# Optimization experiments

Hardware: AMD Instinct MI355X
Metric: run time of the kernel (lower is better)

Reference implementation:

```python
import jax, jax.numpy as jnp
import numpy as np

D_IN = 4096
NUM_HEADS = 32
HEAD_DIM = 128
NUM_KV = 8
GROUP = NUM_HEADS // NUM_KV
EPS = 1e-6
ROPE_BASE = 10000.0


def rms_norm(x, scale):
    # norm over last dim (head_dim), computed in fp32 as in torch ref
    var = jnp.mean(x * x, axis=-1, keepdims=True)
    return x * jax.lax.rsqrt(var + EPS) * scale


def rope_cos_sin(positions, dim):
    inv_freq = 1.0 / (ROPE_BASE ** (jnp.arange(0, dim, 2, dtype=jnp.float32) / dim))
    angles = positions.astype(jnp.float32)[:, None] * inv_freq[None, :]  # (N, dim/2)
    angles = jnp.concatenate([angles, angles], axis=-1)  # (N, dim)
    return jnp.cos(angles), jnp.sin(angles)


def apply_rope(t, cos, sin):
    # t: (N, heads, D); cos/sin: (N, D)
    half = t.shape[-1] // 2
    rot = jnp.concatenate([-t[..., half:], t[..., :half]], axis=-1)
    return t * cos[:, None, :] + rot * sin[:, None, :]


def setup_inputs() -> dict:
    key = jax.random.key(0)
    ks = jax.random.split(key, 6)
    B, S = 1, 2048
    x = jax.random.normal(ks[0], (B, S, D_IN), dtype=jnp.float32)
    positions = jnp.arange(B * S, dtype=jnp.int32)
    sc = 0.02
    Wq = jax.random.normal(ks[1], (D_IN, NUM_HEADS * HEAD_DIM), dtype=jnp.float32) * sc
    Wk = jax.random.normal(ks[2], (D_IN, NUM_KV * HEAD_DIM), dtype=jnp.float32) * sc
    Wv = jax.random.normal(ks[3], (D_IN, NUM_KV * HEAD_DIM), dtype=jnp.float32) * sc
    Wo = jax.random.normal(ks[4], (NUM_HEADS * HEAD_DIM, D_IN), dtype=jnp.float32) * sc
    q_scale = jnp.ones((HEAD_DIM,), dtype=jnp.float32)
    k_scale = jnp.ones((HEAD_DIM,), dtype=jnp.float32)
    return {"x": x, "positions": positions, "Wq": Wq, "Wk": Wk, "Wv": Wv,
            "Wo": Wo, "q_scale": q_scale, "k_scale": k_scale}


def reference(x, positions, Wq, Wk, Wv, Wo, q_scale, k_scale):
    B, S, _ = x.shape
    N = B * S
    xf = x.reshape(N, D_IN)
    q = (xf @ Wq).reshape(N, NUM_HEADS, HEAD_DIM)
    k = (xf @ Wk).reshape(N, NUM_KV, HEAD_DIM)
    v = (xf @ Wv).reshape(N, NUM_KV, HEAD_DIM)
    # QK RMSNorm over head_dim
    q = rms_norm(q, q_scale)
    k = rms_norm(k, k_scale)
    # RoPE (rotate-half)
    cos, sin = rope_cos_sin(positions, HEAD_DIM)
    q = apply_rope(q, cos, sin)
    k = apply_rope(k, cos, sin)
    # (B, KV, group, S, D) for q; (B, KV, S, D) for k, v  (GQA broadcast)
    q = q.reshape(B, S, NUM_KV, GROUP, HEAD_DIM).transpose(0, 2, 3, 1, 4)
    k = k.reshape(B, S, NUM_KV, HEAD_DIM).transpose(0, 2, 1, 3)
    v = v.reshape(B, S, NUM_KV, HEAD_DIM).transpose(0, 2, 1, 3)
    scale = 1.0 / jnp.sqrt(jnp.float32(HEAD_DIM))
    scores = jnp.einsum('bghsd,bgtd->bghst', q, k) * scale  # (B,KV,G,S,S)
    causal = jnp.tril(jnp.ones((S, S), dtype=bool))
    scores = jnp.where(causal[None, None, None, :, :], scores, jnp.finfo(scores.dtype).min)
    attn = jax.nn.softmax(scores, axis=-1)
    ctx = jnp.einsum('bghst,bgtd->bghsd', attn, v)  # (B,KV,G,S,D)
    ctx = ctx.transpose(0, 3, 1, 2, 4).reshape(B, S, NUM_HEADS * HEAD_DIM)
    return ctx @ Wo
```

## Files before the change

kernel.cpp:

```cpp
#include <hip/hip_runtime.h>

#define S_LEN 2048
#define DMODEL 4096
#define NQKV 6144

typedef unsigned short u16;
typedef __attribute__((ext_vector_type(8))) short bf16x8;
typedef __attribute__((ext_vector_type(8))) unsigned short u16x8;
typedef __attribute__((ext_vector_type(4))) float f32x4;

#define NEG_BIG (-3.0e38f)

__device__ __forceinline__ float bf2f(u16 h) {
    union { unsigned u; float f; } c; c.u = ((unsigned)h) << 16; return c.f;
}
__device__ __forceinline__ u16 f2bf(float x) {
    union { float f; unsigned u; } c; c.f = x;
    return (u16)((c.u + 0x7fffu + ((c.u >> 16) & 1u)) >> 16);
}

__device__ __forceinline__ void gload16(const void* g, void* l) {
    __builtin_amdgcn_global_load_lds(
        (const __attribute__((address_space(1))) void*)g,
        (__attribute__((address_space(3))) void*)l, 16, 0, 0);
}

__device__ __forceinline__ void barfence() {
    asm volatile("" ::: "memory");
    __builtin_amdgcn_s_barrier();
    asm volatile("" ::: "memory");
}

#define MFMA16(d, av, bv) d = __builtin_amdgcn_mfma_f32_16x16x32_bf16(av, bv, d, 0, 0, 0)

__global__ __launch_bounds__(256) void detect_dtype(const u16* __restrict__ probe,
                                                    int* __restrict__ flags) {
    __shared__ int bad_s;
    if (threadIdx.x == 0) bad_s = 0;
    __syncthreads();
    int bad = 0;
    for (int i = threadIdx.x; i < 16384; i += 256) {
        float v = bf2f(probe[i]);
        if (!(fabsf(v) < 1e6f)) bad = 1;
    }
    if (bad) atomicOr(&bad_s, 1);
    __syncthreads();
    if (threadIdx.x == 0) { flags[0] = bad_s; flags[1] = 0; }
}

__global__ __launch_bounds__(256) void conv_bf16(const void* __restrict__ src,
                                                 u16* __restrict__ dst, long n,
                                                 const int* __restrict__ flag) {
    const bool f32 = (*flag != 0);
    long i = (long)blockIdx.x * 256 + threadIdx.x;
    long stride = (long)gridDim.x * 256;
    for (; i < n; i += stride) {
        float v = f32 ? ((const float*)src)[i] : bf2f(((const u16*)src)[i]);
        dst[i] = f2bf(v);
    }
}

__global__ __launch_bounds__(256) void transpose_any(
        const void* __restrict__ src, long base_off, long sld, long szoff,
        u16* __restrict__ dst, long dld, long dzoff,
        const int* __restrict__ flag) {
    __shared__ alignas(16) u16 tile[32][33];
    const bool f32 = (*flag != 0);
    u16* d = dst + (long)blockIdx.z * dzoff;
    long soff = base_off + (long)blockIdx.z * szoff;
    int c0 = blockIdx.x * 32, r0 = blockIdx.y * 32;
    int tx = threadIdx.x & 31, ty = threadIdx.x >> 5;
    for (int i = 0; i < 32; i += 8) {
        long idx = soff + (long)(r0 + ty + i) * sld + c0 + tx;
        float v = f32 ? ((const float*)src)[idx] : bf2f(((const u16*)src)[idx]);
        tile[ty + i][tx] = f2bf(v);
    }
    __syncthreads();
    for (int i = 0; i < 32; i += 8)
        d[(long)(c0 + ty + i) * dld + r0 + tx] = tile[tx][ty + i];
}

__global__ __launch_bounds__(512, 2) void gemm_dp4_bf16(
        const u16* __restrict__ A, const u16* __restrict__ BT,
        u16* __restrict__ C, int K, int ldc) {
    __shared__ alignas(16) u16 smem[57344];
    const int tid = threadIdx.x;
    const int lane = tid & 63, wid = tid >> 6;
    const int wr = wid >> 2, wc = wid & 3;
    const int lm = lane & 15, lq = lane >> 4;
    const int m0 = blockIdx.y * 256, n0 = blockIdx.x * 192;

    const int srow = tid >> 3;
    const int sgrp = (tid & 7) ^ (srow & 7);
    const u16* aS = A  + (size_t)(m0 + srow) * K + sgrp * 8;
    const u16* bS = BT + (size_t)(n0 + srow) * K + sgrp * 8;
    u16* ldsA = smem + tid * 8;
    u16* ldsB = smem + 16384 + tid * 8;

    auto stA = [&](int bufi, int c, int kti) {
        gload16(aS + (size_t)c * 64 * K + (size_t)kti * 64, ldsA + bufi * 28672 + c * 4096);
    };
    auto stB = [&](int bufi, int c, int kti) {
        gload16(bS + (size_t)c * 64 * K + (size_t)kti * 64, ldsB + bufi * 28672 + c * 4096);
    };
    auto rdA = [&](const u16* buf, int mi, int ks) {
        int row = wr * 128 + mi * 16 + lm;
        return *(const bf16x8*)(const void*)(buf + row * 64 + (((ks * 4 + lq) ^ (row & 7)) << 3));
    };
    auto rdB = [&](const u16* buf, int ni, int ks) {
        int row = wc * 48 + ni * 16 + lm;
        return *(const bf16x8*)(const void*)(buf + 16384 + row * 64 + (((ks * 4 + lq) ^ (row & 7)) << 3));
    };

    const int NK = K >> 6;
    stB(0, 0, 0); stB(0, 1, 0); stB(0, 2, 0);
    stA(0, 0, 0); stA(0, 2, 0); stA(0, 1, 0); stA(0, 3, 0);

    f32x4 acc[8][3] = {};
    bf16x8 b[3][2], a[2][2];

#pragma unroll 2
    for (int kt = 0; kt < NK; ++kt) {
        const u16* buf = smem + (kt & 1) * 28672;
        const int nb = (kt & 1) ^ 1;
        const int kn = kt + 1;
        const bool more = kn < NK;

        asm volatile("s_waitcnt vmcnt(2)" ::: "memory");
        barfence();
#pragma unroll
        for (int ni = 0; ni < 3; ++ni)
#pragma unroll
            for (int ks = 0; ks < 2; ++ks) b[ni][ks] = rdB(buf, ni, ks);
#pragma unroll
        for (int q = 0; q < 2; ++q)
#pragma unroll
            for (int ks = 0; ks < 2; ++ks) a[q][ks] = rdA(buf, q, ks);
        if (more) { stB(nb, 0, kn); stB(nb, 1, kn); stB(nb, 2, kn); }
        __builtin_amdgcn_s_setprio(1);
#pragma unroll
        for (int q = 0; q < 2; ++q)
#pragma unroll
            for (int ni = 0; ni < 3; ++ni)
#pragma unroll
                for (int ks = 0; ks < 2; ++ks) MFMA16(acc[q][ni], a[q][ks], b[ni][ks]);
        __builtin_amdgcn_s_setprio(0);

#pragma unroll
        for (int q = 0; q < 2; ++q)
#pragma unroll
            for (int ks = 0; ks < 2; ++ks) a[q][ks] = rdA(buf, 2 + q, ks);
        if (more) { stA(nb, 0, kn); stA(nb, 2, kn); }
        __builtin_amdgcn_s_setprio(1);
#pragma unroll
        for (int q = 0; q < 2; ++q)
#pragma unroll
            for (int ni = 0; ni < 3; ++ni)
#pragma unroll
                for (int ks = 0; ks < 2; ++ks) MFMA16(acc[2 + q][ni], a[q][ks], b[ni][ks]);
        __builtin_amdgcn_s_setprio(0);

        if (more) { asm volatile("s_waitcnt vmcnt(5)" ::: "memory"); }
        else      { asm volatile("s_waitcnt vmcnt(0)" ::: "memory"); }
        barfence();
#pragma unroll
        for (int q = 0; q < 2; ++q)
#pragma unroll
            for (int ks = 0; ks < 2; ++ks) a[q][ks] = rdA(buf, 4 + q, ks);
        if (more) { stA(nb, 1, kn); stA(nb, 3, kn); }
        __builtin_amdgcn_s_setprio(1);
#pragma unroll
        for (int q = 0; q < 2; ++q)
#pragma unroll
            for (int ni = 0; ni < 3; ++ni)
#pragma unroll
                for (int ks = 0; ks < 2; ++ks) MFMA16(acc[4 + q][ni], a[q][ks], b[ni][ks]);
        __builtin_amdgcn_s_setprio(0);

#pragma unroll
        for (int q = 0; q < 2; ++q)
#pragma unroll
            for (int ks = 0; ks < 2; ++ks) a[q][ks] = rdA(buf, 6 + q, ks);
        __builtin_amdgcn_s_setprio(1);
#pragma unroll
        for (int q = 0; q < 2; ++q)
#pragma unroll
            for (int ni = 0; ni < 3; ++ni)
#pragma unroll
                for (int ks = 0; ks < 2; ++ks) MFMA16(acc[6 + q][ni], a[q][ks], b[ni][ks]);
        __builtin_amdgcn_s_setprio(0);
    }

#pragma unroll
    for (int mi = 0; mi < 8; ++mi)
#pragma unroll
        for (int ni = 0; ni < 3; ++ni) {
            int col  = n0 + wc * 48 + ni * 16 + lm;
            int rowb = m0 + wr * 128 + mi * 16 + lq * 4;
#pragma unroll
            for (int r = 0; r < 4; ++r)
                C[(size_t)(rowb + r) * ldc + col] = f2bf(acc[mi][ni][r]);
        }
}

__global__ __launch_bounds__(512, 2) void gemm_dp3_f32(
        const u16* __restrict__ A, const u16* __restrict__ BT,
        float* __restrict__ C, int K, int ldc) {
    __shared__ alignas(16) u16 smem[49152];
    const int tid = threadIdx.x;
    const int lane = tid & 63, wid = tid >> 6;
    const int wr = wid >> 1, wc = wid & 1;
    const int lm = lane & 15, lq = lane >> 4;
    const int m0 = blockIdx.y * 128, n0 = blockIdx.x * 256;

    const int srow = tid >> 3;
    const int sgrp = (tid & 7) ^ (srow & 7);
    const u16* aS = A  + (size_t)(m0 + srow) * K + sgrp * 8;
    const u16* bS = BT + (size_t)(n0 + srow) * K + sgrp * 8;
    u16* ldsA = smem + tid * 8;
    u16* ldsB = smem + 8192 + tid * 8;

    auto stA = [&](int bufi, int c, int kti) {
        gload16(aS + (size_t)c * 64 * K + (size_t)kti * 64, ldsA + bufi * 24576 + c * 4096);
    };
    auto stB = [&](int bufi, int c, int kti) {
        gload16(bS + (size_t)c * 64 * K + (size_t)kti * 64, ldsB + bufi * 24576 + c * 4096);
    };
    auto rdA = [&](const u16* buf, int mi, int ks) {
        int row = wr * 32 + mi * 16 + lm;
        return *(const bf16x8*)(const void*)(buf + row * 64 + (((ks * 4 + lq) ^ (row & 7)) << 3));
    };
    auto rdB = [&](const u16* buf, int ni, int ks) {
        int row = wc * 128 + ni * 16 + lm;
        return *(const bf16x8*)(const void*)(buf + 8192 + row * 64 + (((ks * 4 + lq) ^ (row & 7)) << 3));
    };

    const int NK = K >> 6;
    stA(0, 0, 0); stA(0, 1, 0); stB(0, 0, 0); stB(0, 2, 0);
    stB(0, 1, 0); stB(0, 3, 0);

    f32x4 acc[2][8] = {};
    bf16x8 a[2][2], b[4][2];

#pragma unroll 2
    for (int kt = 0; kt < NK; ++kt) {
        const u16* buf = smem + (kt & 1) * 24576;
        const int nb = (kt & 1) ^ 1;
        const int kn = kt + 1;
        const bool more = kn < NK;

        asm volatile("s_waitcnt vmcnt(2)" ::: "memory");
        barfence();
#pragma unroll
        for (int mi = 0; mi < 2; ++mi)
#pragma unroll
            for (int ks = 0; ks < 2; ++ks) a[mi][ks] = rdA(buf, mi, ks);
#pragma unroll
        for (int ni = 0; ni < 4; ++ni)
#pragma unroll
            for (int ks = 0; ks < 2; ++ks) b[ni][ks] = rdB(buf, ni, ks);
        if (more) { stA(nb, 0, kn); stA(nb, 1, kn); stB(nb, 0, kn); stB(nb, 2, kn); }
        __builtin_amdgcn_s_setprio(1);
#pragma unroll
        for (int mi = 0; mi < 2; ++mi)
#pragma unroll
            for (int ni = 0; ni < 4; ++ni)
#pragma unroll
                for (int ks = 0; ks < 2; ++ks) MFMA16(acc[mi][ni], a[mi][ks], b[ni][ks]);
        __builtin_amdgcn_s_setprio(0);

        if (more) { asm volatile("s_waitcnt vmcnt(4)" ::: "memory"); }
        else      { asm volatile("s_waitcnt vmcnt(0)" ::: "memory"); }
        barfence();
#pragma unroll
        for (int ni = 0; ni < 4; ++ni)
#pragma unroll
            for (int ks = 0; ks < 2; ++ks) b[ni][ks] = rdB(buf, 4 + ni, ks);
        if (more) { stB(nb, 1, kn); stB(nb, 3, kn); }
        __builtin_amdgcn_s_setprio(1);
#pragma unroll
        for (int mi = 0; mi < 2; ++mi)
#pragma unroll
            for (int ni = 0; ni < 4; ++ni)
#pragma unroll
                for (int ks = 0; ks < 2; ++ks) MFMA16(acc[mi][4 + ni], a[mi][ks], b[ni][ks]);
        __builtin_amdgcn_s_setprio(0);
    }

#pragma unroll
    for (int mi = 0; mi < 2; ++mi)
#pragma unroll
        for (int ni = 0; ni < 8; ++ni) {
            int col  = n0 + wc * 128 + ni * 16 + lm;
            int rowb = m0 + wr * 32 + mi * 16 + lq * 4;
#pragma unroll
            for (int r = 0; r < 4; ++r)
                C[(size_t)(rowb + r) * ldc + col] = acc[mi][ni][r];
        }
}

__global__ __launch_bounds__(256) void rms_rope(
        const u16* __restrict__ qkv, const int* __restrict__ pos,
        const u16* __restrict__ qs, const u16* __restrict__ kscale,
        u16* __restrict__ Qb, u16* __restrict__ Kb) {
    int w = threadIdx.x >> 6, lane = threadIdx.x & 63;
    int task = blockIdx.x * 4 + w;
    int h = task >> 11, row = task & 2047;
    int base = (h < 32) ? h * 128 : 4096 + (h - 32) * 128;
    const u16* src = qkv + (size_t)row * NQKV + base;
    float t0 = bf2f(src[lane]), t1 = bf2f(src[lane + 64]);
    float ss = t0 * t0 + t1 * t1;
    for (int m = 1; m < 64; m <<= 1) ss += __shfl_xor(ss, m);
    float inv = rsqrtf(ss * (1.0f / 128.0f) + 1e-6f);
    const u16* sc = (h < 32) ? qs : kscale;
    float n0 = t0 * inv * bf2f(sc[lane]);
    float n1 = t1 * inv * bf2f(sc[lane + 64]);
    float p = (float)pos[row];
    float ang = p * __expf(-(float)lane * (9.210340371976184f / 64.0f));
    float c = cosf(ang), s = sinf(ang);
    float o0 = n0 * c - n1 * s;
    float o1 = n1 * c + n0 * s;
    float mul = (h < 32) ? 0.08838834764831845f : 1.0f;
    u16* dst = (h < 32) ? (Qb + ((size_t)h * S_LEN + row) * 128)
                        : (Kb + ((size_t)(h - 32) * S_LEN + row) * 128);
    dst[lane] = f2bf(o0 * mul);
    dst[lane + 64] = f2bf(o1 * mul);
}

__global__ __launch_bounds__(256, 2) void flash_attn(
        const u16* __restrict__ Qb, const u16* __restrict__ Kb,
        const u16* __restrict__ VTb, u16* __restrict__ ctx) {
    const int h = blockIdx.y, kvh = h >> 2;
    const int tid = threadIdx.x, lane = tid & 63, w = tid >> 6;
    const int lm = lane & 15, lq = lane >> 4;
    const int swz = (lm & 7) << 3;
    __shared__ alignas(16) u16 smem[36864];
    u16* Psm = smem + 32768;
    const u16* Kh = Kb + (size_t)kvh * S_LEN * 128;
    const u16* Vh = VTb + (size_t)kvh * 128 * S_LEN;

    auto stageK = [&](int j) {
        for (int i = 0; i < 4; ++i) {
            int g = i * 256 + tid;
            int row = g >> 4, s = g & 15;
            int sp = (s & 8) | ((s ^ row) & 7);
            gload16(Kh + (size_t)(j * 64 + row) * 128 + sp * 8,
                    smem + (j & 1) * 8192 + (size_t)(i * 256 + w * 64) * 8);
        }
    };
    auto stageV = [&](int j) {
        for (int i = 0; i < 4; ++i) {
            int g = i * 256 + tid;
            int d = g >> 3, s = g & 7;
            int sp = s ^ (d & 7);
            gload16(Vh + (size_t)d * S_LEN + j * 64 + sp * 8,
                    smem + 16384 + (j & 1) * 8192 + (size_t)(i * 256 + w * 64) * 8);
        }
    };

    for (int pass = 0; pass < 2; ++pass) {
        const int t = pass ? (31 - blockIdx.x) : blockIdx.x;
        const u16* Qh = Qb + ((size_t)h * S_LEN + (size_t)t * 64) * 128;

        barfence();
        for (int i = 0; i < 4; ++i) {
            int g = i * 256 + tid;
            int row = g >> 4, s = g & 15;
            int sp = (s & 8) | ((s ^ row) & 7);
            gload16(Qh + (size_t)row * 128 + sp * 8,
                    smem + (size_t)(i * 256 + w * 64) * 8);
        }
        asm volatile("s_waitcnt vmcnt(0)" ::: "memory");
        barfence();
        bf16x8 aq[4];
        for (int ks = 0; ks < 4; ++ks)
            aq[ks] = *(const bf16x8*)(const void*)(
                smem + (((w * 16 + lm) * 128 + ks * 32 + lq * 8) ^ swz));
        asm volatile("s_waitcnt lgkmcnt(0)" ::: "memory");
        barfence();
        stageK(0); stageV(0);

        float mrow[4], lrow[4];
        f32x4 accO[8];
        const f32x4 zero = {0.f, 0.f, 0.f, 0.f};
        for (int r = 0; r < 4; ++r) { mrow[r] = NEG_BIG; lrow[r] = 0.f; }
        for (int di = 0; di < 8; ++di) accO[di] = zero;

        for (int j = 0; j <= t; ++j) {
            const u16* Kj = smem + (j & 1) * 8192;
            const u16* Vj = smem + 16384 + (j & 1) * 8192;
            if (j < t) {
                stageK(j + 1); stageV(j + 1);
                asm volatile("s_waitcnt vmcnt(8)" ::: "memory");
            } else {
                asm volatile("s_waitcnt vmcnt(0)" ::: "memory");
            }
            barfence();

            f32x4 sacc[4] = {};
            for (int ks = 0; ks < 4; ++ks) {
                bf16x8 kf[4];
                for (int ni = 0; ni < 4; ++ni)
                    kf[ni] = *(const bf16x8*)(const void*)(
                        Kj + (((ni * 16 + lm) * 128 + ks * 32 + lq * 8) ^ swz));
                for (int ni = 0; ni < 4; ++ni)
                    sacc[ni] = __builtin_amdgcn_mfma_f32_16x16x32_bf16(aq[ks], kf[ni], sacc[ni], 0, 0, 0);
            }

            if (j == t) {
                for (int ni = 0; ni < 4; ++ni) {
                    int col = ni * 16 + lm;
                    for (int r = 0; r < 4; ++r)
                        if (col > w * 16 + lq * 4 + r) sacc[ni][r] = NEG_BIG;
                }
            }

            for (int r = 0; r < 4; ++r) {
                float mx = fmaxf(fmaxf(sacc[0][r], sacc[1][r]),
                                 fmaxf(sacc[2][r], sacc[3][r]));
                for (int sft = 1; sft < 16; sft <<= 1) mx = fmaxf(mx, __shfl_xor(mx, sft));
                float mN = fmaxf(mrow[r], mx);
                float alpha = __expf(mrow[r] - mN);
                mrow[r] = mN;
                float psum = 0.f;
                int prow = w * 16 + lq * 4 + r;
                for (int ni = 0; ni < 4; ++ni) {
                    float pv = __expf(sacc[ni][r] - mN);
                    psum += pv;
                    Psm[prow * 64 + ((ni * 16 + lm) ^ ((prow & 7) << 3))] = f2bf(pv);
                }
                for (int sft = 1; sft < 16; sft <<= 1) psum += __shfl_xor(psum, sft);
                lrow[r] = lrow[r] * alpha + psum;
                for (int di = 0; di < 8; ++di) accO[di][r] *= alpha;
            }
            asm volatile("s_waitcnt lgkmcnt(0)" ::: "memory");
            barfence();

            for (int ks2 = 0; ks2 < 2; ++ks2) {
                bf16x8 pf = *(const bf16x8*)(const void*)(
                    Psm + (((w * 16 + lm) * 64 + ks2 * 32 + lq * 8) ^ swz));
                for (int di = 0; di < 8; ++di) {
                    bf16x8 vf = *(const bf16x8*)(const void*)(
                        Vj + (((di * 16 + lm) * 64 + ks2 * 32 + lq * 8) ^ swz));
                    accO[di] = __builtin_amdgcn_mfma_f32_16x16x32_bf16(pf, vf, accO[di], 0, 0, 0);
                }
            }
            barfence();
        }

        for (int r = 0; r < 4; ++r) {
            float invl = 1.0f / fmaxf(lrow[r], 1e-30f);
            size_t rowg = (size_t)t * 64 + w * 16 + lq * 4 + r;
            for (int di = 0; di < 8; ++di)
                ctx[rowg * 4096 + h * 128 + di * 16 + lm] = f2bf(accO[di][r] * invl);
        }
    }
}

extern "C" void kernel_launch(void* const* d_in, const int* in_sizes, int n_in,
                              void* d_out, int out_size, void* d_ws, size_t ws_size,
                              hipStream_t stream) {
    const void* x   = d_in[0];
    const int* pos  = (const int*)d_in[1];
    const void* Wq  = d_in[2];
    const void* Wk  = d_in[3];
    const void* Wv  = d_in[4];
    const void* Wo  = d_in[5];
    const void* qs  = d_in[6];
    const void* ks  = d_in[7];

    if (ws_size < (size_t)145 * 1024 * 1024) return;
    char* ws = (char*)d_ws;
    u16* WqkvT = (u16*)ws;
    u16* WoT   = (u16*)(ws + (size_t)48  * 1024 * 1024);
    u16* qkv   = (u16*)(ws + (size_t)80  * 1024 * 1024);
    u16* ctx   = qkv;
    u16* Qb    = (u16*)(ws + (size_t)104 * 1024 * 1024);
    u16* Kb    = (u16*)(ws + (size_t)120 * 1024 * 1024);
    u16* VTb   = (u16*)(ws + (size_t)124 * 1024 * 1024);
    u16* xb    = (u16*)(ws + (size_t)128 * 1024 * 1024);
    int* flags = (int*)(ws + (size_t)144 * 1024 * 1024);
    u16* qsb   = (u16*)(ws + (size_t)144 * 1024 * 1024 + 1024);
    u16* ksb   = (u16*)(ws + (size_t)144 * 1024 * 1024 + 2048);

    dim3 b256(256);
    const int* flag  = flags;
    const int* fzero = flags + 1;

    detect_dtype<<<1, b256, 0, stream>>>((const u16*)Wq, flags);
    conv_bf16<<<8192, b256, 0, stream>>>(x,  xb,  (long)S_LEN * DMODEL, flag);
    conv_bf16<<<1,    b256, 0, stream>>>(qs, qsb, 128, flag);
    conv_bf16<<<1,    b256, 0, stream>>>(ks, ksb, 128, flag);

    transpose_any<<<dim3(128, 128, 1), b256, 0, stream>>>(Wq, 0, 4096, 0, WqkvT, 4096, 0, flag);
    transpose_any<<<dim3(32, 128, 1),  b256, 0, stream>>>(Wk, 0, 1024, 0, WqkvT + (size_t)4096 * 4096, 4096, 0, flag);
    transpose_any<<<dim3(32, 128, 1),  b256, 0, stream>>>(Wv, 0, 1024, 0, WqkvT + (size_t)5120 * 4096, 4096, 0, flag);
    transpose_any<<<dim3(128, 128, 1), b256, 0, stream>>>(Wo, 0, 4096, 0, WoT, 4096, 0, flag);

    gemm_dp4_bf16<<<dim3(32, 8), dim3(512), 0, stream>>>(xb, WqkvT, qkv, 4096, NQKV);
    rms_rope<<<dim3(20480), b256, 0, stream>>>(qkv, pos, qsb, ksb, Qb, Kb);
    transpose_any<<<dim3(4, 64, 8), b256, 0, stream>>>(qkv, 5120, NQKV, 128, VTb, 2048, (long)128 * 2048, fzero);
    flash_attn<<<dim3(16, 32), b256, 0, stream>>>(Qb, Kb, VTb, ctx);
    gemm_dp3_f32<<<dim3(16, 16), dim3(512), 0, stream>>>(ctx, WoT, (float*)d_out, 4096, 4096);
}
```

Baseline: 542.5 us.

## Enlarge flash-attention query tile to 128 rows and add lazy softmax rescaling

```diff
diff --git a/kernel.cpp b/kernel.cpp
--- a/kernel.cpp
+++ b/kernel.cpp
@@ -327,14 +327,14 @@
     dst[lane + 64] = f2bf(o1 * mul);
 }
 
-__global__ __launch_bounds__(256, 2) void flash_attn(
+__global__ __launch_bounds__(256, 1) void flash_attn(
         const u16* __restrict__ Qb, const u16* __restrict__ Kb,
         const u16* __restrict__ VTb, u16* __restrict__ ctx) {
     const int h = blockIdx.y, kvh = h >> 2;
     const int tid = threadIdx.x, lane = tid & 63, w = tid >> 6;
     const int lm = lane & 15, lq = lane >> 4;
     const int swz = (lm & 7) << 3;
-    __shared__ alignas(16) u16 smem[36864];
+    __shared__ alignas(16) u16 smem[40960];
     u16* Psm = smem + 32768;
     const u16* Kh = Kb + (size_t)kvh * S_LEN * 128;
     const u16* Vh = VTb + (size_t)kvh * 128 * S_LEN;
@@ -359,11 +359,11 @@
     };
 
     for (int pass = 0; pass < 2; ++pass) {
-        const int t = pass ? (31 - blockIdx.x) : blockIdx.x;
-        const u16* Qh = Qb + ((size_t)h * S_LEN + (size_t)t * 64) * 128;
-
-        barfence();
-        for (int i = 0; i < 4; ++i) {
+        const int t = pass ? (15 - blockIdx.x) : blockIdx.x;
+        const u16* Qh = Qb + ((size_t)h * S_LEN + (size_t)t * 128) * 128;
+
+        barfence();
+        for (int i = 0; i < 8; ++i) {
             int g = i * 256 + tid;
             int row = g >> 4, s = g & 15;
             int sp = (s & 8) | ((s ^ row) & 7);
@@ -372,24 +372,28 @@
         }
         asm volatile("s_waitcnt vmcnt(0)" ::: "memory");
         barfence();
-        bf16x8 aq[4];
-        for (int ks = 0; ks < 4; ++ks)
-            aq[ks] = *(const bf16x8*)(const void*)(
-                smem + (((w * 16 + lm) * 128 + ks * 32 + lq * 8) ^ swz));
+        bf16x8 aq[2][4];
+        for (int mi = 0; mi < 2; ++mi)
+            for (int ks = 0; ks < 4; ++ks)
+                aq[mi][ks] = *(const bf16x8*)(const void*)(
+                    smem + (((w * 32 + mi * 16 + lm) * 128 + ks * 32 + lq * 8) ^ swz));
         asm volatile("s_waitcnt lgkmcnt(0)" ::: "memory");
         barfence();
         stageK(0); stageV(0);
 
-        float mrow[4], lrow[4];
-        f32x4 accO[8];
+        float mrow[2][4], lrow[2][4];
+        f32x4 accO[2][8];
         const f32x4 zero = {0.f, 0.f, 0.f, 0.f};
-        for (int r = 0; r < 4; ++r) { mrow[r] = NEG_BIG; lrow[r] = 0.f; }
-        for (int di = 0; di < 8; ++di) accO[di] = zero;
-
-        for (int j = 0; j <= t; ++j) {
+        for (int mi = 0; mi < 2; ++mi)
+            for (int r = 0; r < 4; ++r) { mrow[mi][r] = NEG_BIG; lrow[mi][r] = 0.f; }
+        for (int mi = 0; mi < 2; ++mi)
+            for (int di = 0; di < 8; ++di) accO[mi][di] = zero;
+
+        const int jmax = 2 * t + 1;
+        for (int j = 0; j <= jmax; ++j) {
             const u16* Kj = smem + (j & 1) * 8192;
             const u16* Vj = smem + 16384 + (j & 1) * 8192;
-            if (j < t) {
+            if (j < jmax) {
                 stageK(j + 1); stageV(j + 1);
                 asm volatile("s_waitcnt vmcnt(8)" ::: "memory");
             } else {
@@ -397,63 +401,83 @@
             }
             barfence();
 
-            f32x4 sacc[4] = {};
+            f32x4 sacc[2][4] = {};
             for (int ks = 0; ks < 4; ++ks) {
                 bf16x8 kf[4];
                 for (int ni = 0; ni < 4; ++ni)
                     kf[ni] = *(const bf16x8*)(const void*)(
                         Kj + (((ni * 16 + lm) * 128 + ks * 32 + lq * 8) ^ swz));
-                for (int ni = 0; ni < 4; ++ni)
-                    sacc[ni] = __builtin_amdgcn_mfma_f32_16x16x32_bf16(aq[ks], kf[ni], sacc[ni], 0, 0, 0);
+                for (int mi = 0; mi < 2; ++mi)
+                    for (int ni = 0; ni < 4; ++ni)
+                        MFMA16(sacc[mi][ni], aq[mi][ks], kf[ni]);
             }
 
-            if (j == t) {
-                for (int ni = 0; ni < 4; ++ni) {
-                    int col = ni * 16 + lm;
-                    for (int r = 0; r < 4; ++r)
-                        if (col > w * 16 + lq * 4 + r) sacc[ni][r] = NEG_BIG;
+            if (j >= 2 * t) {
+                for (int mi = 0; mi < 2; ++mi)
+                    for (int ni = 0; ni < 4; ++ni) {
+                        int colg = j * 64 + ni * 16 + lm;
+                        int rowg = t * 128 + w * 32 + mi * 16 + lq * 4;
+                        for (int r = 0; r < 4; ++r)
+                            if (colg > rowg + r) sacc[mi][ni][r] = NEG_BIG;
+                    }
+            }
+
+            float mx[2][4];
+            bool need = false;
+            for (int mi = 0; mi < 2; ++mi)
+                for (int r = 0; r < 4; ++r) {
+                    float m0 = fmaxf(fmaxf(sacc[mi][0][r], sacc[mi][1][r]),
+                                     fmaxf(sacc[mi][2][r], sacc[mi][3][r]));
+                    for (int sft = 1; sft < 16; sft <<= 1) m0 = fmaxf(m0, __shfl_xor(m0, sft));
+                    mx[mi][r] = m0;
+                    need = need || (m0 > mrow[mi][r] + 8.0f);
                 }
+            if (__any(need)) {
+                for (int mi = 0; mi < 2; ++mi)
+                    for (int r = 0; r < 4; ++r) {
+                        float mN = fmaxf(mrow[mi][r], mx[mi][r]);
+                        float alpha = __expf(mrow[mi][r] - mN);
+                        mrow[mi][r] = mN;
+                        lrow[mi][r] *= alpha;
+                        for (int di = 0; di < 8; ++di) accO[mi][di][r] *= alpha;
+                    }
             }
-
-            for (int r = 0; r < 4; ++r) {
-                float mx = fmaxf(fmaxf(sacc[0][r], sacc[1][r]),
-                                 fmaxf(sacc[2][r], sacc[3][r]));
-                for (int sft = 1; sft < 16; sft <<= 1) mx = fmaxf(mx, __shfl_xor(mx, sft));
-                float mN = fmaxf(mrow[r], mx);
-                float alpha = __expf(mrow[r] - mN);
-                mrow[r] = mN;
-                float psum = 0.f;
-                int prow = w * 16 + lq * 4 + r;
-                for (int ni = 0; ni < 4; ++ni) {
-                    float pv = __expf(sacc[ni][r] - mN);
-                    psum += pv;
-                    Psm[prow * 64 + ((ni * 16 + lm) ^ ((prow & 7) << 3))] = f2bf(pv);
+            for (int mi = 0; mi < 2; ++mi)
+                for (int r = 0; r < 4; ++r) {
+                    float psum = 0.f;
+                    int prow = w * 32 + mi * 16 + lq * 4 + r;
+                    for (int ni = 0; ni < 4; ++ni) {
+                        float pv = __expf(sacc[mi][ni][r] - mrow[mi][r]);
+                        psum += pv;
+                        Psm[prow * 64 + ((ni * 16 + lm) ^ ((prow & 7) << 3))] = f2bf(pv);
+                    }
+                    for (int sft = 1; sft < 16; sft <<= 1) psum += __shfl_xor(psum, sft);
+                    lrow[mi][r] += psum;
                 }
-                for (int sft = 1; sft < 16; sft <<= 1) psum += __shfl_xor(psum, sft);
-                lrow[r] = lrow[r] * alpha + psum;
-                for (int di = 0; di < 8; ++di) accO[di][r] *= alpha;
-            }
             asm volatile("s_waitcnt lgkmcnt(0)" ::: "memory");
-            barfence();
 
             for (int ks2 = 0; ks2 < 2; ++ks2) {
-                bf16x8 pf = *(const bf16x8*)(const void*)(
-                    Psm + (((w * 16 + lm) * 64 + ks2 * 32 + lq * 8) ^ swz));
+                bf16x8 pf[2];
+                for (int mi = 0; mi < 2; ++mi)
+                    pf[mi] = *(const bf16x8*)(const void*)(
+                        Psm + (((w * 32 + mi * 16 + lm) * 64 + ks2 * 32 + lq * 8) ^ swz));
                 for (int di = 0; di < 8; ++di) {
                     bf16x8 vf = *(const bf16x8*)(const void*)(
                         Vj + (((di * 16 + lm) * 64 + ks2 * 32 + lq * 8) ^ swz));
-                    accO[di] = __builtin_amdgcn_mfma_f32_16x16x32_bf16(pf, vf, accO[di], 0, 0, 0);
+                    for (int mi = 0; mi < 2; ++mi)
+                        MFMA16(accO[mi][di], pf[mi], vf);
                 }
             }
             barfence();
         }
 
-        for (int r = 0; r < 4; ++r) {
-            float invl = 1.0f / fmaxf(lrow[r], 1e-30f);
-            size_t rowg = (size_t)t * 64 + w * 16 + lq * 4 + r;
-            for (int di = 0; di < 8; ++di)
-                ctx[rowg * 4096 + h * 128 + di * 16 + lm] = f2bf(accO[di][r] * invl);
-        }
+        for (int mi = 0; mi < 2; ++mi)
+            for (int r = 0; r < 4; ++r) {
+                float invl = 1.0f / fmaxf(lrow[mi][r], 1e-30f);
+                size_t rowg = (size_t)t * 128 + w * 32 + mi * 16 + lq * 4 + r;
+                for (int di = 0; di < 8; ++di)
+                    ctx[rowg * 4096 + h * 128 + di * 16 + lm] = f2bf(accO[mi][di][r] * invl);
+            }
     }
 }
 
@@ -500,6 +524,6 @@
     gemm_dp4_bf16<<<dim3(32, 8), dim3(512), 0, stream>>>(xb, WqkvT, qkv, 4096, NQKV);
     rms_rope<<<dim3(20480), b256, 0, stream>>>(qkv, pos, qsb, ksb, Qb, Kb);
     transpose_any<<<dim3(4, 64, 8), b256, 0, stream>>>(qkv, 5120, NQKV, 128, VTb, 2048, (long)128 * 2048, fzero);
-    flash_attn<<<dim3(16, 32), b256, 0, stream>>>(Qb, Kb, VTb, ctx);
+    flash_attn<<<dim3(8, 32), b256, 0, stream>>>(Qb, Kb, VTb, ctx);
     gemm_dp3_f32<<<dim3(16, 16), dim3(512), 0, stream>>>(ctx, WoT, (float*)d_out, 4096, 4096);
 }
```

Result: slower. 577.6 us (+6.5%).
